# Performance work log

Hardware: AMD Instinct MI355X
Metric: run time of the kernel (lower is better)

## Reference

```python
import jax, jax.numpy as jnp
import numpy as np

N = 100000      # nodes
E = 1600000     # edges (avg degree 16)
IN, HID, OUT = 64, 64, 32
R = 8           # relations


def setup_inputs() -> dict:
    key = jax.random.key(0)
    ks = jax.random.split(key, 8)
    s = jnp.float32(0.05)  # weight init scale
    return {
        "feat": jax.random.normal(ks[0], (N, IN), dtype=jnp.float32),
        "src": jax.random.randint(ks[1], (E,), 0, N),
        "dst": jax.random.randint(ks[2], (E,), 0, N),
        "etypes": jax.random.randint(ks[3], (E,), 0, R),
        "W1": jax.random.normal(ks[4], (R, IN, HID), dtype=jnp.float32) * s,
        "Wself1": jax.random.normal(ks[5], (IN, HID), dtype=jnp.float32) * s,
        "b1": jnp.zeros((HID,), jnp.float32),
        "W2": jax.random.normal(ks[6], (R, HID, OUT), dtype=jnp.float32) * s,
        "Wself2": jax.random.normal(ks[7], (HID, OUT), dtype=jnp.float32) * s,
        "b2": jnp.zeros((OUT,), jnp.float32),
    }


def _rel_graph_conv(h, src, dst, etypes, W, Wself, b):
    """RelGraphConv with sum aggregation, self-loop and bias.

    h: [N, din], W: [R, din, dout], Wself: [din, dout], b: [dout].
    """
    n = h.shape[0]
    # Transform all nodes by all relation weights once: [R, N, dout].
    hW = jnp.einsum('nd,rdo->rno', h, W)
    # Per-edge message: relation-specific transform of the source node.
    msg = hW[etypes, src]                                    # [E, dout]
    # Scatter-add messages to destination nodes.
    agg = jax.ops.segment_sum(msg, dst, num_segments=n)      # [N, dout]
    return agg + h @ Wself + b


def reference(feat, src, dst, etypes, W1, Wself1, b1, W2, Wself2, b2):
    x = jax.nn.relu(_rel_graph_conv(feat, src, dst, etypes, W1, Wself1, b1))
    return _rel_graph_conv(x, src, dst, etypes, W2, Wself2, b2)
```

## Files before the change

kernel.cpp:

```cpp
#include <hip/hip_runtime.h>
#include <hip/hip_bf16.h>

typedef __attribute__((ext_vector_type(8))) short short8;
typedef __attribute__((ext_vector_type(4))) float f32x4;

__device__ __forceinline__ unsigned short f2bf(float v) {
    __hip_bfloat16 h = __float2bfloat16(v);
    return *reinterpret_cast<unsigned short*>(&h);
}
__device__ __forceinline__ float bf2f(unsigned short u) {
    union { unsigned int i; float f; } x;
    x.i = (unsigned int)u << 16;
    return x.f;
}

constexpr int MAXB = 2048;

template<int H>
__global__ __launch_bounds__(256) void transpose_w(
    const float* __restrict__ W, const float* __restrict__ Wself,
    unsigned short* __restrict__ Wt, int R)
{
    int i = blockIdx.x * 256 + threadIdx.x;
    int total = (R + 1) * H * 64;
    if (i >= total) return;
    int d = i & 63;
    int hh = i >> 6;
    int r = hh / H, h = hh % H;
    float v = (r < R) ? W[((size_t)r * 64 + d) * H + h]
                      : Wself[(size_t)d * H + h];
    Wt[i] = f2bf(v);
}

template<int H, int RT>
__global__ __launch_bounds__(512) void gemm_rel_mfma(
    const float* __restrict__ A, const unsigned short* __restrict__ Wt,
    const float* __restrict__ bias,
    unsigned short* __restrict__ C, float* __restrict__ Cself,
    int N, int Rrt, int relu)
{
    constexpr int AS = 72;
    __shared__ unsigned short As[64 * AS];
    const int R = RT ? RT : Rrt;
    const int tid = threadIdx.x;
    const int n0 = blockIdx.x * 64;

    #pragma unroll
    for (int i = 0; i < 2; ++i) {
        int lin = tid + i * 512;
        int n = lin >> 4;
        int d4 = (lin & 15) * 4;
        int gn = n0 + n;
        float4 v = make_float4(0.f, 0.f, 0.f, 0.f);
        if (gn < N) v = *(const float4*)&A[(size_t)gn * 64 + d4];
        if (relu) {
            v.x = fmaxf(v.x, 0.f); v.y = fmaxf(v.y, 0.f);
            v.z = fmaxf(v.z, 0.f); v.w = fmaxf(v.w, 0.f);
        }
        ushort4 u;
        u.x = f2bf(v.x); u.y = f2bf(v.y); u.z = f2bf(v.z); u.w = f2bf(v.w);
        *(ushort4*)&As[n * AS + d4] = u;
    }

    const int w = tid >> 6, lane = tid & 63;
    const int m = lane & 15, quad = lane >> 4;
    const int wt = w & 3;
    const int half = w >> 2;

    __syncthreads();

    short8 afrag[2];
    afrag[0] = *(const short8*)&As[(wt * 16 + m) * AS + 0 * 32 + quad * 8];
    afrag[1] = *(const short8*)&As[(wt * 16 + m) * AS + 1 * 32 + quad * 8];

    constexpr int NT = H / 32;
    #pragma unroll
    for (int r = 0; r <= R; ++r) {
        f32x4 acc[NT];
        #pragma unroll
        for (int nt = 0; nt < NT; ++nt) {
            const int colbase = half * (H / 2) + nt * 16;
            acc[nt] = (f32x4){0.f, 0.f, 0.f, 0.f};
            #pragma unroll
            for (int kc = 0; kc < 2; ++kc) {
                short8 bfrag = *(const short8*)
                    &Wt[((size_t)(r * H + colbase + m)) * 64 + kc * 32 + quad * 8];
                acc[nt] = __builtin_amdgcn_mfma_f32_16x16x32_bf16(afrag[kc], bfrag, acc[nt], 0, 0, 0);
            }
        }
        if (r < R) {
            #pragma unroll
            for (int nt = 0; nt < NT; ++nt) {
                int col = half * (H / 2) + nt * 16 + m;
                #pragma unroll
                for (int i = 0; i < 4; ++i) {
                    int node = n0 + wt * 16 + quad * 4 + i;
                    if (node < N)
                        C[((size_t)r * N + node) * H + col] = f2bf(acc[nt][i]);
                }
            }
        } else {
            #pragma unroll
            for (int nt = 0; nt < NT; ++nt) {
                int col = half * (H / 2) + nt * 16 + m;
                float bv = bias[col];
                #pragma unroll
                for (int i = 0; i < 4; ++i) {
                    int node = n0 + wt * 16 + quad * 4 + i;
                    if (node < N)
                        Cself[(size_t)node * H + col] = acc[nt][i] + bv;
                }
            }
        }
    }
}

__global__ __launch_bounds__(256) void zero_int(int* __restrict__ p, int n) {
    int i = blockIdx.x * 256 + threadIdx.x;
    if (i < n) p[i] = 0;
}

__global__ __launch_bounds__(256) void fine_hist(
    const int* __restrict__ dst, int* __restrict__ ghist, int E, int B, int CH)
{
    __shared__ int hist[MAXB];
    const int t = threadIdx.x;
    const int e0 = blockIdx.x * CH, e1 = min(E, e0 + CH);
    for (int i = t; i < B; i += 256) hist[i] = 0;
    __syncthreads();
    for (int e = e0 + t; e < e1; e += 256) atomicAdd(&hist[dst[e] >> 6], 1);
    __syncthreads();
    for (int i = t; i < B; i += 256) {
        int h = hist[i];
        if (h) atomicAdd(&ghist[i], h);
    }
}

__global__ __launch_bounds__(256) void fine_scan(
    const int* __restrict__ ghist, int* __restrict__ bstart,
    int* __restrict__ cursor, int B, int E)
{
    __shared__ int ts[256];
    const int t = threadIdx.x;
    const int PER = (B + 255) / 256;
    int loc[8];
    int s = 0;
    for (int j = 0; j < PER; ++j) {
        int i = t * PER + j;
        loc[j] = (i < B) ? ghist[i] : 0;
        s += loc[j];
    }
    ts[t] = s;
    __syncthreads();
    for (int off = 1; off < 256; off <<= 1) {
        int x = (t >= off) ? ts[t - off] : 0;
        __syncthreads();
        ts[t] += x;
        __syncthreads();
    }
    int run = ts[t] - s;
    for (int j = 0; j < PER; ++j) {
        int i = t * PER + j;
        if (i < B) { bstart[i] = run; cursor[i] = run; }
        run += loc[j];
    }
    if (t == 255) bstart[B] = E;
}

__global__ __launch_bounds__(256) void partition_fine(
    const int* __restrict__ src, const int* __restrict__ dst,
    const int* __restrict__ et, int* __restrict__ cursor,
    int* __restrict__ rec, int E, int N, int B, int CH)
{
    __shared__ int hist[MAXB];
    __shared__ int base[MAXB];
    __shared__ int cnt[MAXB];
    const int t = threadIdx.x;
    const int e0 = blockIdx.x * CH, e1 = min(E, e0 + CH);

    for (int i = t; i < B; i += 256) hist[i] = 0;
    __syncthreads();
    for (int e = e0 + t; e < e1; e += 256) atomicAdd(&hist[dst[e] >> 6], 1);
    __syncthreads();
    for (int i = t; i < B; i += 256) {
        int h = hist[i];
        base[i] = h ? atomicAdd(&cursor[i], h) : 0;
        cnt[i] = 0;
    }
    __syncthreads();
    for (int e = e0 + t; e < e1; e += 256) {
        int d = dst[e];
        int b = d >> 6;
        int pos = base[b] + atomicAdd(&cnt[b], 1);
        rec[pos] = ((et[e] * N + src[e]) << 6) | (d & 63);
    }
}

__global__ __launch_bounds__(256) void bucket_sort(
    const int* __restrict__ bstart, const int* __restrict__ rec,
    int* __restrict__ eidx, int* __restrict__ row_ptr, int N, int E)
{
    __shared__ int hist[64];
    __shared__ int excl[64];
    __shared__ int cur[64];
    const int b = blockIdx.x;
    const int tid = threadIdx.x;
    const int p0 = bstart[b], p1 = bstart[b + 1];

    if (tid < 64) hist[tid] = 0;
    __syncthreads();
    for (int p = p0 + tid; p < p1; p += 256)
        atomicAdd(&hist[rec[p] & 63], 1);
    __syncthreads();
    if (tid == 0) {
        int run = 0;
        #pragma unroll
        for (int i = 0; i < 64; ++i) { excl[i] = run; run += hist[i]; }
    }
    __syncthreads();
    if (tid < 64) {
        cur[tid] = excl[tid];
        int n = b * 64 + tid;
        if (n < N) row_ptr[n] = p0 + excl[tid];
    }
    if (b == 0 && tid == 0) row_ptr[N] = E;
    __syncthreads();
    for (int p = p0 + tid; p < p1; p += 256) {
        int rv = rec[p];
        int pos = p0 + atomicAdd(&cur[rv & 63], 1);
        eidx[pos] = rv >> 6;
    }
}

template<int F>
__global__ __launch_bounds__(256) void agg_csr(
    const unsigned short* __restrict__ hW, const int* __restrict__ row_ptr,
    const int* __restrict__ eidx, float* __restrict__ out, int N)
{
    constexpr int G = 256 / F;
    const int d = blockIdx.x * G + threadIdx.x / F;
    const int lane = threadIdx.x % F;
    if (d >= N) return;
    const int p1 = row_ptr[d + 1];
    int p = row_ptr[d];
    float a0 = 0.f, a1 = 0.f, a2 = 0.f, a3 = 0.f;
    for (; p + 7 < p1; p += 8) {
        int i0 = eidx[p],     i1 = eidx[p + 1], i2 = eidx[p + 2], i3 = eidx[p + 3];
        int i4 = eidx[p + 4], i5 = eidx[p + 5], i6 = eidx[p + 6], i7 = eidx[p + 7];
        a0 += bf2f(hW[(size_t)i0 * F + lane]);
        a1 += bf2f(hW[(size_t)i1 * F + lane]);
        a2 += bf2f(hW[(size_t)i2 * F + lane]);
        a3 += bf2f(hW[(size_t)i3 * F + lane]);
        a0 += bf2f(hW[(size_t)i4 * F + lane]);
        a1 += bf2f(hW[(size_t)i5 * F + lane]);
        a2 += bf2f(hW[(size_t)i6 * F + lane]);
        a3 += bf2f(hW[(size_t)i7 * F + lane]);
    }
    for (; p + 1 < p1; p += 2) {
        int i0 = eidx[p], i1 = eidx[p + 1];
        a0 += bf2f(hW[(size_t)i0 * F + lane]);
        a1 += bf2f(hW[(size_t)i1 * F + lane]);
    }
    if (p < p1) a0 += bf2f(hW[(size_t)eidx[p] * F + lane]);
    out[(size_t)d * F + lane] += (a0 + a1) + (a2 + a3);
}

extern "C" void kernel_launch(void* const* d_in, const int* in_sizes, int n_in,
                              void* d_out, int out_size, void* d_ws, size_t ws_size,
                              hipStream_t stream)
{
    const float* feat = (const float*)d_in[0];
    const int*   src  = (const int*)d_in[1];
    const int*   dst  = (const int*)d_in[2];
    const int*   et   = (const int*)d_in[3];
    const float* W1   = (const float*)d_in[4];
    const float* Ws1  = (const float*)d_in[5];
    const float* b1   = (const float*)d_in[6];
    const float* W2   = (const float*)d_in[7];
    const float* Ws2  = (const float*)d_in[8];
    const float* b2   = (const float*)d_in[9];
    float* out = (float*)d_out;

    const int N = in_sizes[0] / 64;
    const int E = in_sizes[1];
    const int R = in_sizes[4] / (64 * 64);
    const int B = (N + 63) / 64;

    unsigned short* hW  = (unsigned short*)d_ws;
    float* h1      = (float*)(hW + (size_t)R * N * 64);
    unsigned short* Wt1 = (unsigned short*)(h1 + (size_t)N * 64);
    unsigned short* Wt2 = Wt1 + (size_t)(R + 1) * 64 * 64;
    int*   ghist   = (int*)(Wt2 + (size_t)(R + 1) * 32 * 64);
    int*   bstart  = ghist + B;
    int*   cursor  = bstart + (B + 1);
    int*   row_ptr = cursor + B;
    int*   rec     = row_ptr + (N + 1);
    int*   eidx    = rec + E;

    const dim3 blk(256);
    const int nblk64 = (N + 63) / 64;
    const int P  = 128;
    const int CH = (E + P - 1) / P;

    transpose_w<64><<<((R + 1) * 64 * 64 + 255) / 256, blk, 0, stream>>>(W1, Ws1, Wt1, R);
    transpose_w<32><<<((R + 1) * 32 * 64 + 255) / 256, blk, 0, stream>>>(W2, Ws2, Wt2, R);

    zero_int<<<(B + 255) / 256, blk, 0, stream>>>(ghist, B);
    fine_hist<<<P, blk, 0, stream>>>(dst, ghist, E, B, CH);
    fine_scan<<<1, blk, 0, stream>>>(ghist, bstart, cursor, B, E);
    partition_fine<<<P, blk, 0, stream>>>(src, dst, et, cursor, rec, E, N, B, CH);
    bucket_sort<<<B, blk, 0, stream>>>(bstart, rec, eidx, row_ptr, N, E);

    if (R == 8)
        gemm_rel_mfma<64, 8><<<nblk64, 512, 0, stream>>>(feat, Wt1, b1, hW, h1, N, R, 0);
    else
        gemm_rel_mfma<64, 0><<<nblk64, 512, 0, stream>>>(feat, Wt1, b1, hW, h1, N, R, 0);
    agg_csr<64><<<dim3((N + 3) / 4), blk, 0, stream>>>(hW, row_ptr, eidx, h1, N);

    if (R == 8)
        gemm_rel_mfma<32, 8><<<nblk64, 512, 0, stream>>>(h1, Wt2, b2, hW, out, N, R, 1);
    else
        gemm_rel_mfma<32, 0><<<nblk64, 512, 0, stream>>>(h1, Wt2, b2, hW, out, N, R, 1);
    agg_csr<32><<<dim3((N + 7) / 8), blk, 0, stream>>>(hW, row_ptr, eidx, out, N);
}
```

Measured before the change: 398.9 us.

## Swap MFMA operands for vectorized row stores and prefetch weight fragments

```diff
diff --git a/kernel.cpp b/kernel.cpp
--- a/kernel.cpp
+++ b/kernel.cpp
@@ -66,6 +66,7 @@
     const int m = lane & 15, quad = lane >> 4;
     const int wt = w & 3;
     const int half = w >> 2;
+    const int node = n0 + wt * 16 + m;
 
     __syncthreads();
 
@@ -74,43 +75,65 @@
     afrag[1] = *(const short8*)&As[(wt * 16 + m) * AS + 1 * 32 + quad * 8];
 
     constexpr int NT = H / 32;
+
+    auto wptr = [&](int r, int nt, int kc) {
+        int colbase = half * (H / 2) + nt * 16;
+        return (const short8*)&Wt[((size_t)(r * H + colbase + m)) * 64 + kc * 32 + quad * 8];
+    };
+
+    short8 wf0[NT][2], wf1[NT][2];
+    #pragma unroll
+    for (int nt = 0; nt < NT; ++nt) { wf0[nt][0] = *wptr(0, nt, 0); wf0[nt][1] = *wptr(0, nt, 1); }
+    #pragma unroll
+    for (int nt = 0; nt < NT; ++nt) { wf1[nt][0] = *wptr(1, nt, 0); wf1[nt][1] = *wptr(1, nt, 1); }
+
     #pragma unroll
     for (int r = 0; r <= R; ++r) {
+        short8 wn[NT][2];
+        if (r + 2 <= R) {
+            #pragma unroll
+            for (int nt = 0; nt < NT; ++nt) {
+                wn[nt][0] = *wptr(r + 2, nt, 0);
+                wn[nt][1] = *wptr(r + 2, nt, 1);
+            }
+        }
+
         f32x4 acc[NT];
         #pragma unroll
         for (int nt = 0; nt < NT; ++nt) {
-            const int colbase = half * (H / 2) + nt * 16;
             acc[nt] = (f32x4){0.f, 0.f, 0.f, 0.f};
-            #pragma unroll
-            for (int kc = 0; kc < 2; ++kc) {
-                short8 bfrag = *(const short8*)
-                    &Wt[((size_t)(r * H + colbase + m)) * 64 + kc * 32 + quad * 8];
-                acc[nt] = __builtin_amdgcn_mfma_f32_16x16x32_bf16(afrag[kc], bfrag, acc[nt], 0, 0, 0);
-            }
-        }
+            acc[nt] = __builtin_amdgcn_mfma_f32_16x16x32_bf16(wf0[nt][0], afrag[0], acc[nt], 0, 0, 0);
+            acc[nt] = __builtin_amdgcn_mfma_f32_16x16x32_bf16(wf0[nt][1], afrag[1], acc[nt], 0, 0, 0);
+        }
+
         if (r < R) {
             #pragma unroll
             for (int nt = 0; nt < NT; ++nt) {
-                int col = half * (H / 2) + nt * 16 + m;
-                #pragma unroll
-                for (int i = 0; i < 4; ++i) {
-                    int node = n0 + wt * 16 + quad * 4 + i;
-                    if (node < N)
-                        C[((size_t)r * N + node) * H + col] = f2bf(acc[nt][i]);
+                int colbase = half * (H / 2) + nt * 16;
+                if (node < N) {
+                    ushort4 u;
+                    u.x = f2bf(acc[nt][0]); u.y = f2bf(acc[nt][1]);
+                    u.z = f2bf(acc[nt][2]); u.w = f2bf(acc[nt][3]);
+                    *(ushort4*)&C[((size_t)r * N + node) * H + colbase + quad * 4] = u;
                 }
             }
         } else {
             #pragma unroll
             for (int nt = 0; nt < NT; ++nt) {
-                int col = half * (H / 2) + nt * 16 + m;
-                float bv = bias[col];
-                #pragma unroll
-                for (int i = 0; i < 4; ++i) {
-                    int node = n0 + wt * 16 + quad * 4 + i;
-                    if (node < N)
-                        Cself[(size_t)node * H + col] = acc[nt][i] + bv;
+                int colbase = half * (H / 2) + nt * 16;
+                if (node < N) {
+                    float4 bv = *(const float4*)&bias[colbase + quad * 4];
+                    float4 o = make_float4(acc[nt][0] + bv.x, acc[nt][1] + bv.y,
+                                           acc[nt][2] + bv.z, acc[nt][3] + bv.w);
+                    *(float4*)&Cself[(size_t)node * H + colbase + quad * 4] = o;
                 }
             }
+        }
+
+        #pragma unroll
+        for (int nt = 0; nt < NT; ++nt) {
+            wf0[nt][0] = wf1[nt][0]; wf0[nt][1] = wf1[nt][1];
+            wf1[nt][0] = wn[nt][0];  wf1[nt][1] = wn[nt][1];
         }
     }
 }
```

Result: no change. 394.2 us (-1.2%).
